# Kernel tuning notes

Measured on AMD Instinct MI355X. Metric: run time of the kernel, lower is better.

Reference implementation:

```python
import jax, jax.numpy as jnp
import numpy as np

B, S, F, H = 8, 2048, 512, 4
W = 32            # local window size
DH = F // H       # head dim
EPS = 1e-5


def layer_norm(x, w, b):
    mu = jnp.mean(x, axis=-1, keepdims=True)
    var = jnp.var(x, axis=-1, keepdims=True)
    return (x - mu) * jax.lax.rsqrt(var + EPS) * w + b


def mha(x, w_in, b_in, w_out, b_out):
    # x: [..., L, F]; torch nn.MultiheadAttention self-attention (dropout inactive / eval)
    qkv = x @ w_in.T + b_in                      # [..., L, 3F]
    q, k, v = jnp.split(qkv, 3, axis=-1)
    lead = x.shape[:-2]
    L = x.shape[-2]

    def heads(t):  # [..., L, F] -> [..., H, L, DH]
        return jnp.swapaxes(t.reshape(*lead, L, H, DH), -3, -2)

    q, k, v = heads(q), heads(k), heads(v)
    scores = jnp.einsum('...hld,...hmd->...hlm', q, k) / np.sqrt(DH)
    p = jax.nn.softmax(scores, axis=-1)
    o = jnp.einsum('...hlm,...hmd->...hld', p, v)  # [..., H, L, DH]
    o = jnp.swapaxes(o, -3, -2).reshape(*lead, L, F)
    return o @ w_out.T + b_out


def setup_inputs() -> dict:
    key = jax.random.key(0)
    ks = jax.random.split(key, 16)
    s = 0.02
    p = lambda k, shape: jax.random.normal(k, shape, dtype=jnp.float32) * s
    return {
        'x': jax.random.normal(ks[0], (B, S, F), dtype=jnp.float32),
        'l_in_w': p(ks[1], (3 * F, F)), 'l_in_b': p(ks[2], (3 * F,)),
        'l_out_w': p(ks[3], (F, F)),   'l_out_b': p(ks[4], (F,)),
        'g_in_w': p(ks[5], (3 * F, F)), 'g_in_b': p(ks[6], (3 * F,)),
        'g_out_w': p(ks[7], (F, F)),   'g_out_b': p(ks[8], (F,)),
        'n1_w': jnp.ones((F,)), 'n1_b': jnp.zeros((F,)),
        'n2_w': jnp.ones((F,)), 'n2_b': jnp.zeros((F,)),
        'gate_w': p(ks[9], (F, 2 * F)), 'gate_b': p(ks[10], (F,)),
        'gln_w': jnp.ones((F,)), 'gln_b': jnp.zeros((F,)),
    }


def reference(x, l_in_w, l_in_b, l_out_w, l_out_b,
              g_in_w, g_in_b, g_out_w, g_out_b,
              n1_w, n1_b, n2_w, n2_b,
              gate_w, gate_b, gln_w, gln_b):
    # local branch: block-diagonal (windowed) self-attention, all windows batched
    xw = x.reshape(B, S // W, W, F)
    local = mha(xw, l_in_w, l_in_b, l_out_w, l_out_b).reshape(B, S, F)
    local = layer_norm(x + local, n1_w, n1_b)
    # global branch: full self-attention
    glob = mha(x, g_in_w, g_in_b, g_out_w, g_out_b)
    glob = layer_norm(x + glob, n2_w, n2_b)
    # learned gate fusion
    gi = jnp.concatenate([local, glob], axis=-1)
    gate = jax.nn.sigmoid(layer_norm(gi @ gate_w.T + gate_b, gln_w, gln_b))
    return gate * local + (1.0 - gate) * glob
```

## Files before the change

### kernel.cpp

```cpp
#include <hip/hip_runtime.h>
#include <stdint.h>

#define BB 8
#define SS 2048
#define FF 512
#define HH 4
#define TOK (BB * SS)

typedef unsigned short u16;
typedef short short8 __attribute__((ext_vector_type(8)));
typedef float f32x4 __attribute__((ext_vector_type(4)));
typedef float f32x16 __attribute__((ext_vector_type(16)));
typedef unsigned int u32x4 __attribute__((ext_vector_type(4)));

static __device__ __forceinline__ u16 f2bf(float f) {
  uint32_t u = __builtin_bit_cast(uint32_t, f);
  u = (u + 0x7fffu + ((u >> 16) & 1u)) >> 16;
  return (u16)u;
}
static __device__ __forceinline__ float bf2f(u16 u) {
  return __builtin_bit_cast(float, (uint32_t)u << 16);
}

static __device__ __forceinline__ uint32_t cvtpk(float lo, float hi) {
  uint32_t r;
  asm("v_cvt_pk_bf16_f32 %0, %1, %2" : "=v"(r) : "v"(lo), "v"(hi));
  return r;
}

static __device__ __forceinline__ void cp16(void* lds, const void* g) {
  __builtin_amdgcn_global_load_lds(
      (const __attribute__((address_space(1))) void*)g,
      (__attribute__((address_space(3))) void*)lds, 16, 0, 0);
}

__global__ __launch_bounds__(256) void castk(const float* __restrict__ s,
                                             u16* __restrict__ d, int n) {
  const int i = (blockIdx.x * 256 + threadIdx.x) * 8;
  if (i >= n) return;
  float4 a = *(const float4*)(s + i);
  float4 b = *(const float4*)(s + i + 4);
  short8 o;
  o[0] = (short)f2bf(a.x); o[1] = (short)f2bf(a.y);
  o[2] = (short)f2bf(a.z); o[3] = (short)f2bf(a.w);
  o[4] = (short)f2bf(b.x); o[5] = (short)f2bf(b.y);
  o[6] = (short)f2bf(b.z); o[7] = (short)f2bf(b.w);
  *(short8*)(d + i) = o;
}

__global__ __launch_bounds__(256) void gemm_bt(
    const u16* __restrict__ A, const u16* __restrict__ B,
    const float* __restrict__ bias, float* __restrict__ Cf,
    u16* __restrict__ Cb, int M, int N, int K, int qcols, float qscale) {
  const int m0 = blockIdx.x << 7;
  const int n0 = blockIdx.y << 7;
  __shared__ u16 As[128 * 64];
  __shared__ u16 Bs[128 * 64];
  const int tid = threadIdx.x;
  const int wave = tid >> 6, lane = tid & 63;
  const int wr = wave >> 1, wc = wave & 1;

  f32x4 acc[4][4];
#pragma unroll
  for (int i = 0; i < 4; ++i)
#pragma unroll
    for (int j = 0; j < 4; ++j)
#pragma unroll
      for (int e = 0; e < 4; ++e) acc[i][j][e] = 0.f;

  for (int k0 = 0; k0 < K; k0 += 64) {
#pragma unroll
    for (int i = 0; i < 4; ++i) {
      const int base = (i * 4 + wave) << 10;
      const int lb = base + (lane << 4);
      const int r = lb >> 7;
      const int s = ((lb >> 4) & 7) ^ (r & 7);
      cp16((char*)As + base, A + (size_t)(m0 + r) * K + k0 + s * 8);
      cp16((char*)Bs + base, B + (size_t)(n0 + r) * K + k0 + s * 8);
    }
    __syncthreads();
#pragma unroll
    for (int kk = 0; kk < 2; ++kk) {
      short8 af[4], bfr[4];
#pragma unroll
      for (int mi = 0; mi < 4; ++mi) {
        const int r = wr * 64 + mi * 16 + (lane & 15);
        const int p = (kk * 4 + (lane >> 4)) ^ (r & 7);
        af[mi] = *(const short8*)(As + r * 64 + p * 8);
      }
#pragma unroll
      for (int ni = 0; ni < 4; ++ni) {
        const int r = wc * 64 + ni * 16 + (lane & 15);
        const int p = (kk * 4 + (lane >> 4)) ^ (r & 7);
        bfr[ni] = *(const short8*)(Bs + r * 64 + p * 8);
      }
#pragma unroll
      for (int mi = 0; mi < 4; ++mi)
#pragma unroll
        for (int ni = 0; ni < 4; ++ni)
          acc[mi][ni] = __builtin_amdgcn_mfma_f32_16x16x32_bf16(
              af[mi], bfr[ni], acc[mi][ni], 0, 0, 0);
    }
    __syncthreads();
  }
  const int rv = (lane >> 4) << 2;
  const int cn = lane & 15;
#pragma unroll
  for (int mi = 0; mi < 4; ++mi)
#pragma unroll
    for (int ni = 0; ni < 4; ++ni) {
      const int gn = n0 + wc * 64 + ni * 16 + cn;
      const float bv = bias ? bias[gn] : 0.f;
      const float sc = (gn < qcols) ? qscale : 1.f;
#pragma unroll
      for (int v = 0; v < 4; ++v) {
        const int gm = m0 + wr * 64 + mi * 16 + rv + v;
        const size_t off = (size_t)gm * N + gn;
        const float val = (acc[mi][ni][v] + bv) * sc;
        if (Cf) Cf[off] = val;
        if (Cb) Cb[off] = f2bf(val);
      }
    }
}

__global__ __launch_bounds__(256) void transpose_v(
    const u16* __restrict__ qkv, u16* __restrict__ vt) {
  const int bh = blockIdx.x, st = blockIdx.y, dt = blockIdx.z;
  const int b = bh >> 2, h = bh & 3;
  __shared__ u16 t[64][72];
  const int r = threadIdx.x >> 3;
  const int c8 = (threadIdx.x & 7) * 8;
#pragma unroll
  for (int ph = 0; ph < 2; ++ph) {
    const int srow = ph * 32 + r;
    const u16* src = qkv + (size_t)(b * SS + st * 64 + srow) * 1536 + 1024 +
                     h * 128 + dt * 64 + c8;
    *(short8*)&t[srow][c8] = *(const short8*)src;
  }
  __syncthreads();
#pragma unroll
  for (int ph = 0; ph < 2; ++ph) {
    const int drow = ph * 32 + r;
    short8 o;
#pragma unroll
    for (int j = 0; j < 8; ++j) o[j] = (short)t[c8 + j][drow];
    *(short8*)(vt + ((size_t)bh * 128 + dt * 64 + drow) * SS + st * 64 + c8) = o;
  }
}

template <typename GET>
static __device__ __forceinline__ short8 make_pa(int ks, GET get) {
  const int c0 = (2 * ks) & 3;
  u32x4 pw;
#pragma unroll
  for (int t = 0; t < 2; ++t) {
    uint32_t a = cvtpk(get(4 * c0 + 2 * t), get(4 * c0 + 2 * t + 1));
    uint32_t b = cvtpk(get(4 * (c0 + 1) + 2 * t), get(4 * (c0 + 1) + 2 * t + 1));
    auto r = __builtin_amdgcn_permlane32_swap(a, b, false, false);
    pw[t] = r[0];
    pw[2 + t] = r[1];
  }
  return __builtin_bit_cast(short8, pw);
}

__global__ __launch_bounds__(256) void attn_local(
    const u16* __restrict__ qkv, const u16* __restrict__ vt,
    u16* __restrict__ ao) {
  const int wave = threadIdx.x >> 6, lane = threadIdx.x & 63;
  const int u = blockIdx.x * 4 + wave;
  const int b = u >> 8, w = (u >> 2) & 63, h = u & 3;
  const int q = lane & 31, half = lane >> 5;

  const size_t qbase = (size_t)(b * SS + w * 32 + q) * 1536 + h * 128;
  short8 qf[8];
#pragma unroll
  for (int d8 = 0; d8 < 8; ++d8)
    qf[d8] = *(const short8*)(qkv + qbase + d8 * 16 + half * 8);

  f32x16 s;
#pragma unroll
  for (int e = 0; e < 16; ++e) s[e] = 0.f;
  const size_t kbase = qbase + 512;
#pragma unroll
  for (int d8 = 0; d8 < 8; ++d8) {
    short8 kf = *(const short8*)(qkv + kbase + d8 * 16 + half * 8);
    s = __builtin_amdgcn_mfma_f32_32x32x16_bf16(kf, qf[d8], s, 0, 0, 0);
  }
  float m = s[0];
#pragma unroll
  for (int e = 1; e < 16; ++e) m = fmaxf(m, s[e]);
  m = fmaxf(m, __shfl_xor(m, 32));
  float l = 0.f;
#pragma unroll
  for (int e = 0; e < 16; ++e) { s[e] = exp2f(s[e] - m); l += s[e]; }
  l += __shfl_xor(l, 32);

  f32x16 o[4];
#pragma unroll
  for (int nt = 0; nt < 4; ++nt)
#pragma unroll
    for (int e = 0; e < 16; ++e) o[nt][e] = 0.f;
  const size_t vbase = ((size_t)(b * 4 + h) * 128) * SS + w * 32;
#pragma unroll
  for (int ks = 0; ks < 2; ++ks) {
    short8 pa = make_pa(ks, [&](int e) { return s[e]; });
#pragma unroll
    for (int nt = 0; nt < 4; ++nt) {
      short8 vb = *(const short8*)(vt + vbase + (size_t)(nt * 32 + q) * SS +
                                   ks * 16 + half * 8);
      o[nt] = __builtin_amdgcn_mfma_f32_32x32x16_bf16(pa, vb, o[nt], 0, 0, 0);
    }
  }
  const float rl = 1.f / l;
  const size_t ob = (size_t)(b * SS + w * 32) * FF + h * 128;
#pragma unroll
  for (int e = 0; e < 16; ++e) {
    const int qr = (e & 3) + 8 * (e >> 2) + 4 * half;
    const float rf = __shfl(rl, qr);
#pragma unroll
    for (int nt = 0; nt < 4; ++nt)
      ao[ob + (size_t)qr * FF + nt * 32 + q] = f2bf(o[nt][e] * rf);
  }
}

__global__ __launch_bounds__(256) void attn_global(
    const u16* __restrict__ qkv, const u16* __restrict__ vt,
    u16* __restrict__ ao) {
  const int lb = (blockIdx.x & 7) * 64 + (blockIdx.x >> 3);
  const int bh = lb >> 4, qt = lb & 15;
  const int b = bh >> 2, h = bh & 3;
  const int wave = threadIdx.x >> 6, lane = threadIdx.x & 63;
  const int q = lane & 31, half = lane >> 5;

  __shared__ u16 Ks[2][64 * 128];
  __shared__ u16 Vs[2][128 * 64];

  short8 qf[8];
  const size_t qb = (size_t)(b * SS + qt * 128 + wave * 32 + q) * 1536 + h * 128;
#pragma unroll
  for (int d8 = 0; d8 < 8; ++d8)
    qf[d8] = *(const short8*)(qkv + qb + d8 * 16 + half * 8);

  f32x16 o[4];
#pragma unroll
  for (int nt = 0; nt < 4; ++nt)
#pragma unroll
    for (int e = 0; e < 16; ++e) o[nt][e] = 0.f;
  float m = -3e38f, lsum = 0.f;

  const size_t kbase = (size_t)b * SS * 1536 + 512 + h * 128;
  const size_t vbase = (size_t)bh * 128 * SS;

  auto STAGE = [&](int kt, int bsel) {
    u16* kd = Ks[bsel];
    u16* vd = Vs[bsel];
#pragma unroll
    for (int i = 0; i < 4; ++i) {
      const int base = (i * 4 + wave) << 10;
      const int lbk = base + (lane << 4);
      {
        const int r = lbk >> 8;
        const int sl = ((lbk >> 4) & 15) ^ (r & 7);
        cp16((char*)kd + base,
             qkv + kbase + (size_t)(kt * 64 + r) * 1536 + sl * 8);
      }
      {
        const int d = lbk >> 7;
        const int sl = ((lbk >> 4) & 7) ^ (d & 7);
        cp16((char*)vd + base, vt + vbase + (size_t)d * SS + kt * 64 + sl * 8);
      }
    }
  };
  STAGE(0, 0);
  __syncthreads();
  for (int kt = 0; kt < 32; ++kt) {
    const int cur = kt & 1;
    if (kt + 1 < 32) STAGE(kt + 1, cur ^ 1);
    const u16* Kb = Ks[cur];
    const u16* Vb = Vs[cur];

    f32x16 sa[2];
#pragma unroll
    for (int mt = 0; mt < 2; ++mt)
#pragma unroll
      for (int e = 0; e < 16; ++e) sa[mt][e] = 0.f;
    __builtin_amdgcn_s_setprio(1);
#pragma unroll
    for (int mt = 0; mt < 2; ++mt) {
      const int kr = mt * 32 + q;
#pragma unroll
      for (int d8 = 0; d8 < 8; ++d8) {
        const int ps = (d8 * 2 + half) ^ (kr & 7);
        short8 kf = *(const short8*)(Kb + kr * 128 + ps * 8);
        sa[mt] = __builtin_amdgcn_mfma_f32_32x32x16_bf16(kf, qf[d8], sa[mt], 0, 0, 0);
      }
    }
    __builtin_amdgcn_s_setprio(0);
    float t[16];
#pragma unroll
    for (int e = 0; e < 16; ++e) t[e] = fmaxf(sa[0][e], sa[1][e]);
#pragma unroll
    for (int st = 8; st >= 1; st >>= 1)
#pragma unroll
      for (int e = 0; e < 8; ++e)
        if (e < st) t[e] = fmaxf(t[e], t[e + st]);
    float pmax = fmaxf(t[0], __shfl_xor(t[0], 32));
    if (__any(pmax > m + 8.f)) {
      const float mn = fmaxf(m, pmax);
      const float corr = exp2f(m - mn);
      m = mn;
      lsum *= corr;
#pragma unroll
      for (int e = 0; e < 16; ++e) {
        const float cf = __shfl(corr, (e & 3) + 8 * (e >> 2) + 4 * half);
#pragma unroll
        for (int nt = 0; nt < 4; ++nt) o[nt][e] *= cf;
      }
    }
#pragma unroll
    for (int mt = 0; mt < 2; ++mt)
#pragma unroll
      for (int e = 0; e < 16; ++e) sa[mt][e] = exp2f(sa[mt][e] - m);
    float u[16];
#pragma unroll
    for (int e = 0; e < 16; ++e) u[e] = sa[0][e] + sa[1][e];
#pragma unroll
    for (int st = 8; st >= 1; st >>= 1)
#pragma unroll
      for (int e = 0; e < 8; ++e)
        if (e < st) u[e] += u[e + st];
    lsum += u[0] + __shfl_xor(u[0], 32);
    __builtin_amdgcn_s_setprio(1);
#pragma unroll
    for (int ks = 0; ks < 4; ++ks) {
      const int mt = ks >> 1;
      short8 pa = make_pa(ks, [&](int e) { return sa[mt][e]; });
#pragma unroll
      for (int nt = 0; nt < 4; ++nt) {
        const int d = nt * 32 + q;
        const int ps = (ks * 2 + half) ^ (d & 7);
        short8 vb = *(const short8*)(Vb + d * 64 + ps * 8);
        o[nt] = __builtin_amdgcn_mfma_f32_32x32x16_bf16(pa, vb, o[nt], 0, 0, 0);
      }
    }
    __builtin_amdgcn_s_setprio(0);
    __syncthreads();
  }
  const float rl = 1.f / lsum;
  const size_t ob = (size_t)(b * SS + qt * 128 + wave * 32) * FF + h * 128;
#pragma unroll
  for (int e = 0; e < 16; ++e) {
    const int qr = (e & 3) + 8 * (e >> 2) + 4 * half;
    const float rf = __shfl(rl, qr);
#pragma unroll
    for (int nt = 0; nt < 4; ++nt)
      ao[ob + (size_t)qr * FF + nt * 32 + q] = f2bf(o[nt][e] * rf);
  }
}

__global__ __launch_bounds__(256) void resid_ln(
    const u16* __restrict__ yb, const float* __restrict__ x,
    const float* __restrict__ w, const float* __restrict__ bv_,
    u16* __restrict__ lg) {
  const int wave = threadIdx.x >> 6, lane = threadIdx.x & 63;
  const size_t row = (size_t)blockIdx.x * 4 + wave;
  const int c = lane * 8;
  const u16* yr = yb + row * FF;
  const float* xr = x + row * FF;
  float v[8];
  {
    short8 a = *(const short8*)(yr + c);
    float4 b0 = *(const float4*)(xr + c), b1 = *(const float4*)(xr + c + 4);
    v[0] = bf2f((u16)a[0]) + b0.x; v[1] = bf2f((u16)a[1]) + b0.y;
    v[2] = bf2f((u16)a[2]) + b0.z; v[3] = bf2f((u16)a[3]) + b0.w;
    v[4] = bf2f((u16)a[4]) + b1.x; v[5] = bf2f((u16)a[5]) + b1.y;
    v[6] = bf2f((u16)a[6]) + b1.z; v[7] = bf2f((u16)a[7]) + b1.w;
  }
  float s = 0.f, s2 = 0.f;
#pragma unroll
  for (int e = 0; e < 8; ++e) { s += v[e]; s2 += v[e] * v[e]; }
#pragma unroll
  for (int off = 1; off < 64; off <<= 1) {
    s += __shfl_xor(s, off);
    s2 += __shfl_xor(s2, off);
  }
  const float mu = s * (1.f / 512.f);
  const float var = s2 * (1.f / 512.f) - mu * mu;
  const float rs = rsqrtf(var + 1e-5f);
  float4 w0 = *(const float4*)(w + c), w1 = *(const float4*)(w + c + 4);
  float4 b0 = *(const float4*)(bv_ + c), b1 = *(const float4*)(bv_ + c + 4);
  const float wv[8] = {w0.x, w0.y, w0.z, w0.w, w1.x, w1.y, w1.z, w1.w};
  const float bb[8] = {b0.x, b0.y, b0.z, b0.w, b1.x, b1.y, b1.z, b1.w};
  short8 ob;
#pragma unroll
  for (int e = 0; e < 8; ++e)
    ob[e] = (short)f2bf((v[e] - mu) * rs * wv[e] + bb[e]);
  *(short8*)(lg + row * 1024 + c) = ob;
}

__global__ __launch_bounds__(256) void gate_final(
    const float* __restrict__ gp, const u16* __restrict__ lg,
    const float* __restrict__ w, const float* __restrict__ bv_,
    float* __restrict__ out) {
  const int wave = threadIdx.x >> 6, lane = threadIdx.x & 63;
  const size_t row = (size_t)blockIdx.x * 4 + wave;
  const int c = lane * 8;
  const float* gr = gp + row * FF;
  float v[8];
  {
    float4 a0 = *(const float4*)(gr + c), a1 = *(const float4*)(gr + c + 4);
    v[0] = a0.x; v[1] = a0.y; v[2] = a0.z; v[3] = a0.w;
    v[4] = a1.x; v[5] = a1.y; v[6] = a1.z; v[7] = a1.w;
  }
  float s = 0.f, s2 = 0.f;
#pragma unroll
  for (int e = 0; e < 8; ++e) { s += v[e]; s2 += v[e] * v[e]; }
#pragma unroll
  for (int off = 1; off < 64; off <<= 1) {
    s += __shfl_xor(s, off);
    s2 += __shfl_xor(s2, off);
  }
  const float mu = s * (1.f / 512.f);
  const float var = s2 * (1.f / 512.f) - mu * mu;
  const float rs = rsqrtf(var + 1e-5f);
  float4 w0 = *(const float4*)(w + c), w1 = *(const float4*)(w + c + 4);
  float4 b0 = *(const float4*)(bv_ + c), b1 = *(const float4*)(bv_ + c + 4);
  const float wv[8] = {w0.x, w0.y, w0.z, w0.w, w1.x, w1.y, w1.z, w1.w};
  const float bb[8] = {b0.x, b0.y, b0.z, b0.w, b1.x, b1.y, b1.z, b1.w};
  short8 l8 = *(const short8*)(lg + row * 1024 + c);
  short8 g8 = *(const short8*)(lg + row * 1024 + 512 + c);
  float r[8];
#pragma unroll
  for (int e = 0; e < 8; ++e) {
    const float z = (v[e] - mu) * rs * wv[e] + bb[e];
    const float gt = 1.f / (1.f + exp2f(-1.44269504f * z));
    r[e] = gt * bf2f((u16)l8[e]) + (1.f - gt) * bf2f((u16)g8[e]);
  }
  *(float4*)(out + row * FF + c) = make_float4(r[0], r[1], r[2], r[3]);
  *(float4*)(out + row * FF + c + 4) = make_float4(r[4], r[5], r[6], r[7]);
}

extern "C" void kernel_launch(void* const* d_in, const int* in_sizes, int n_in,
                              void* d_out, int out_size, void* d_ws,
                              size_t ws_size, hipStream_t stream) {
  const float* x       = (const float*)d_in[0];
  const float* l_in_w  = (const float*)d_in[1];
  const float* l_in_b  = (const float*)d_in[2];
  const float* l_out_w = (const float*)d_in[3];
  const float* l_out_b = (const float*)d_in[4];
  const float* g_in_w  = (const float*)d_in[5];
  const float* g_in_b  = (const float*)d_in[6];
  const float* g_out_w = (const float*)d_in[7];
  const float* g_out_b = (const float*)d_in[8];
  const float* n1_w    = (const float*)d_in[9];
  const float* n1_b    = (const float*)d_in[10];
  const float* n2_w    = (const float*)d_in[11];
  const float* n2_b    = (const float*)d_in[12];
  const float* gate_w  = (const float*)d_in[13];
  const float* gate_b  = (const float*)d_in[14];
  const float* gln_w   = (const float*)d_in[15];
  const float* gln_b   = (const float*)d_in[16];
  float* out = (float*)d_out;

  const float c1 = 0.12752724808f;

  char* ws = (char*)d_ws;
  u16* x_bf  = (u16*)(ws);
  u16* w_liw = (u16*)(ws + 16777216);
  u16* w_giw = (u16*)(ws + 18350080);
  u16* w_low = (u16*)(ws + 19922944);
  u16* w_gow = (u16*)(ws + 20447232);
  u16* w_gt  = (u16*)(ws + 20971520);
  u16* qkv   = (u16*)(ws + 22020096);
  u16* vt    = (u16*)(ws + 72351744);
  u16* ato   = (u16*)(ws + 89128960);
  u16* prj   = (u16*)(ws + 105906176);
  u16* lgbf  = (u16*)(ws + 122683392);
  float* gpre = (float*)(ws + 22020096);

  castk<<<4096, 256, 0, stream>>>(x, x_bf, 8388608);
  castk<<<384, 256, 0, stream>>>(l_in_w, w_liw, 786432);
  castk<<<384, 256, 0, stream>>>(g_in_w, w_giw, 786432);
  castk<<<128, 256, 0, stream>>>(l_out_w, w_low, 262144);
  castk<<<128, 256, 0, stream>>>(g_out_w, w_gow, 262144);
  castk<<<256, 256, 0, stream>>>(gate_w, w_gt, 524288);

  gemm_bt<<<dim3(128, 12), 256, 0, stream>>>(x_bf, w_liw, l_in_b, nullptr, qkv,
                                             TOK, 1536, 512, 512, c1);
  transpose_v<<<dim3(32, 32, 2), 256, 0, stream>>>(qkv, vt);
  attn_local<<<512, 256, 0, stream>>>(qkv, vt, ato);
  gemm_bt<<<dim3(128, 4), 256, 0, stream>>>(ato, w_low, l_out_b, nullptr, prj,
                                            TOK, 512, 512, 0, 1.f);
  resid_ln<<<4096, 256, 0, stream>>>(prj, x, n1_w, n1_b, lgbf);

  gemm_bt<<<dim3(128, 12), 256, 0, stream>>>(x_bf, w_giw, g_in_b, nullptr, qkv,
                                             TOK, 1536, 512, 512, c1);
  transpose_v<<<dim3(32, 32, 2), 256, 0, stream>>>(qkv, vt);
  attn_global<<<512, 256, 0, stream>>>(qkv, vt, ato);
  gemm_bt<<<dim3(128, 4), 256, 0, stream>>>(ato, w_gow, g_out_b, nullptr, prj,
                                            TOK, 512, 512, 0, 1.f);
  resid_ln<<<4096, 256, 0, stream>>>(prj, x, n2_w, n2_b, lgbf + 512);

  gemm_bt<<<dim3(128, 4), 256, 0, stream>>>(lgbf, w_gt, gate_b, gpre, nullptr,
                                            TOK, 512, 1024, 0, 1.f);
  gate_final<<<4096, 256, 0, stream>>>(gpre, lgbf, gln_w, gln_b, out);
}
```

Before: 466.7 us.

## Fuse local and global QKV projections into one GEMM and store gate pre-activation in bf16

The local and global in-projection weights are concatenated so a single 3072-wide GEMM produces both QKV sets into one wider buffer, and all attention and transpose kernels are re-strided to read from it. This removes one kernel launch and gives the GEMM a larger grid. The gate pre-activation GEMM now writes bf16 instead of fp32, which halves that traffic but loses precision before the layer norm. The s_setprio hints around the MFMA sections in global attention are also removed.

```diff
diff --git a/kernel.cpp b/kernel.cpp
--- a/kernel.cpp
+++ b/kernel.cpp
@@ -6,6 +6,7 @@
 #define FF 512
 #define HH 4
 #define TOK (BB * SS)
+#define QST 3072
 
 typedef unsigned short u16;
 typedef short short8 __attribute__((ext_vector_type(8)));
@@ -50,8 +51,9 @@
 
 __global__ __launch_bounds__(256) void gemm_bt(
     const u16* __restrict__ A, const u16* __restrict__ B,
-    const float* __restrict__ bias, float* __restrict__ Cf,
-    u16* __restrict__ Cb, int M, int N, int K, int qcols, float qscale) {
+    const float* __restrict__ bias, const float* __restrict__ bias2,
+    u16* __restrict__ Cb, int M, int N, int K, int nsplit, int qcols,
+    float qscale) {
   const int m0 = blockIdx.x << 7;
   const int n0 = blockIdx.y << 7;
   __shared__ u16 As[128 * 64];
@@ -110,21 +112,19 @@
 #pragma unroll
     for (int ni = 0; ni < 4; ++ni) {
       const int gn = n0 + wc * 64 + ni * 16 + cn;
-      const float bv = bias ? bias[gn] : 0.f;
-      const float sc = (gn < qcols) ? qscale : 1.f;
+      const int cg = (gn >= nsplit) ? gn - nsplit : gn;
+      const float bv = (gn >= nsplit) ? bias2[cg] : bias[cg];
+      const float sc = (cg < qcols) ? qscale : 1.f;
 #pragma unroll
       for (int v = 0; v < 4; ++v) {
         const int gm = m0 + wr * 64 + mi * 16 + rv + v;
-        const size_t off = (size_t)gm * N + gn;
-        const float val = (acc[mi][ni][v] + bv) * sc;
-        if (Cf) Cf[off] = val;
-        if (Cb) Cb[off] = f2bf(val);
+        Cb[(size_t)gm * N + gn] = f2bf((acc[mi][ni][v] + bv) * sc);
       }
     }
 }
 
 __global__ __launch_bounds__(256) void transpose_v(
-    const u16* __restrict__ qkv, u16* __restrict__ vt) {
+    const u16* __restrict__ qkvp, u16* __restrict__ vt) {
   const int bh = blockIdx.x, st = blockIdx.y, dt = blockIdx.z;
   const int b = bh >> 2, h = bh & 3;
   __shared__ u16 t[64][72];
@@ -133,7 +133,7 @@
 #pragma unroll
   for (int ph = 0; ph < 2; ++ph) {
     const int srow = ph * 32 + r;
-    const u16* src = qkv + (size_t)(b * SS + st * 64 + srow) * 1536 + 1024 +
+    const u16* src = qkvp + (size_t)(b * SS + st * 64 + srow) * QST + 1024 +
                      h * 128 + dt * 64 + c8;
     *(short8*)&t[srow][c8] = *(const short8*)src;
   }
@@ -171,7 +171,7 @@
   const int b = u >> 8, w = (u >> 2) & 63, h = u & 3;
   const int q = lane & 31, half = lane >> 5;
 
-  const size_t qbase = (size_t)(b * SS + w * 32 + q) * 1536 + h * 128;
+  const size_t qbase = (size_t)(b * SS + w * 32 + q) * QST + h * 128;
   short8 qf[8];
 #pragma unroll
   for (int d8 = 0; d8 < 8; ++d8)
@@ -236,7 +236,8 @@
   __shared__ u16 Vs[2][128 * 64];
 
   short8 qf[8];
-  const size_t qb = (size_t)(b * SS + qt * 128 + wave * 32 + q) * 1536 + h * 128;
+  const size_t qb =
+      (size_t)(b * SS + qt * 128 + wave * 32 + q) * QST + 1536 + h * 128;
 #pragma unroll
   for (int d8 = 0; d8 < 8; ++d8)
     qf[d8] = *(const short8*)(qkv + qb + d8 * 16 + half * 8);
@@ -248,7 +249,7 @@
     for (int e = 0; e < 16; ++e) o[nt][e] = 0.f;
   float m = -3e38f, lsum = 0.f;
 
-  const size_t kbase = (size_t)b * SS * 1536 + 512 + h * 128;
+  const size_t kbase = (size_t)b * SS * QST + 1536 + 512 + h * 128;
   const size_t vbase = (size_t)bh * 128 * SS;
 
   auto STAGE = [&](int kt, int bsel) {
@@ -262,7 +263,7 @@
         const int r = lbk >> 8;
         const int sl = ((lbk >> 4) & 15) ^ (r & 7);
         cp16((char*)kd + base,
-             qkv + kbase + (size_t)(kt * 64 + r) * 1536 + sl * 8);
+             qkv + kbase + (size_t)(kt * 64 + r) * QST + sl * 8);
       }
       {
         const int d = lbk >> 7;
@@ -284,7 +285,6 @@
     for (int mt = 0; mt < 2; ++mt)
 #pragma unroll
       for (int e = 0; e < 16; ++e) sa[mt][e] = 0.f;
-    __builtin_amdgcn_s_setprio(1);
 #pragma unroll
     for (int mt = 0; mt < 2; ++mt) {
       const int kr = mt * 32 + q;
@@ -295,7 +295,6 @@
         sa[mt] = __builtin_amdgcn_mfma_f32_32x32x16_bf16(kf, qf[d8], sa[mt], 0, 0, 0);
       }
     }
-    __builtin_amdgcn_s_setprio(0);
     float t[16];
 #pragma unroll
     for (int e = 0; e < 16; ++e) t[e] = fmaxf(sa[0][e], sa[1][e]);
@@ -330,7 +329,6 @@
       for (int e = 0; e < 8; ++e)
         if (e < st) u[e] += u[e + st];
     lsum += u[0] + __shfl_xor(u[0], 32);
-    __builtin_amdgcn_s_setprio(1);
 #pragma unroll
     for (int ks = 0; ks < 4; ++ks) {
       const int mt = ks >> 1;
@@ -343,7 +341,6 @@
         o[nt] = __builtin_amdgcn_mfma_f32_32x32x16_bf16(pa, vb, o[nt], 0, 0, 0);
       }
     }
-    __builtin_amdgcn_s_setprio(0);
     __syncthreads();
   }
   const float rl = 1.f / lsum;
@@ -399,18 +396,17 @@
 }
 
 __global__ __launch_bounds__(256) void gate_final(
-    const float* __restrict__ gp, const u16* __restrict__ lg,
+    const u16* __restrict__ gp, const u16* __restrict__ lg,
     const float* __restrict__ w, const float* __restrict__ bv_,
     float* __restrict__ out) {
   const int wave = threadIdx.x >> 6, lane = threadIdx.x & 63;
   const size_t row = (size_t)blockIdx.x * 4 + wave;
   const int c = lane * 8;
-  const float* gr = gp + row * FF;
   float v[8];
   {
-    float4 a0 = *(const float4*)(gr + c), a1 = *(const float4*)(gr + c + 4);
-    v[0] = a0.x; v[1] = a0.y; v[2] = a0.z; v[3] = a0.w;
-    v[4] = a1.x; v[5] = a1.y; v[6] = a1.z; v[7] = a1.w;
+    short8 a = *(const short8*)(gp + row * FF + c);
+#pragma unroll
+    for (int e = 0; e < 8; ++e) v[e] = bf2f((u16)a[e]);
   }
   float s = 0.f, s2 = 0.f;
 #pragma unroll
@@ -466,42 +462,40 @@
 
   char* ws = (char*)d_ws;
   u16* x_bf  = (u16*)(ws);
-  u16* w_liw = (u16*)(ws + 16777216);
-  u16* w_giw = (u16*)(ws + 18350080);
+  u16* w_qkv = (u16*)(ws + 16777216);
   u16* w_low = (u16*)(ws + 19922944);
   u16* w_gow = (u16*)(ws + 20447232);
   u16* w_gt  = (u16*)(ws + 20971520);
-  u16* qkv   = (u16*)(ws + 22020096);
-  u16* vt    = (u16*)(ws + 72351744);
-  u16* ato   = (u16*)(ws + 89128960);
-  u16* prj   = (u16*)(ws + 105906176);
-  u16* lgbf  = (u16*)(ws + 122683392);
-  float* gpre = (float*)(ws + 22020096);
+  u16* qkv2  = (u16*)(ws + 22020096);
+  u16* vt    = (u16*)(ws + 122683392);
+  u16* ato   = (u16*)(ws + 139460608);
+  u16* prj   = (u16*)(ws + 156237824);
+  u16* lgbf  = (u16*)(ws + 173015040);
+  u16* gpre  = (u16*)(ws + 22020096);
 
   castk<<<4096, 256, 0, stream>>>(x, x_bf, 8388608);
-  castk<<<384, 256, 0, stream>>>(l_in_w, w_liw, 786432);
-  castk<<<384, 256, 0, stream>>>(g_in_w, w_giw, 786432);
+  castk<<<384, 256, 0, stream>>>(l_in_w, w_qkv, 786432);
+  castk<<<384, 256, 0, stream>>>(g_in_w, w_qkv + 786432, 786432);
   castk<<<128, 256, 0, stream>>>(l_out_w, w_low, 262144);
   castk<<<128, 256, 0, stream>>>(g_out_w, w_gow, 262144);
   castk<<<256, 256, 0, stream>>>(gate_w, w_gt, 524288);
 
-  gemm_bt<<<dim3(128, 12), 256, 0, stream>>>(x_bf, w_liw, l_in_b, nullptr, qkv,
-                                             TOK, 1536, 512, 512, c1);
-  transpose_v<<<dim3(32, 32, 2), 256, 0, stream>>>(qkv, vt);
-  attn_local<<<512, 256, 0, stream>>>(qkv, vt, ato);
-  gemm_bt<<<dim3(128, 4), 256, 0, stream>>>(ato, w_low, l_out_b, nullptr, prj,
-                                            TOK, 512, 512, 0, 1.f);
+  gemm_bt<<<dim3(128, 24), 256, 0, stream>>>(x_bf, w_qkv, l_in_b, g_in_b, qkv2,
+                                             TOK, 3072, 512, 1536, 512, c1);
+
+  transpose_v<<<dim3(32, 32, 2), 256, 0, stream>>>(qkv2, vt);
+  attn_local<<<512, 256, 0, stream>>>(qkv2, vt, ato);
+  gemm_bt<<<dim3(128, 4), 256, 0, stream>>>(ato, w_low, l_out_b, l_out_b, prj,
+                                            TOK, 512, 512, 512, 0, 1.f);
   resid_ln<<<4096, 256, 0, stream>>>(prj, x, n1_w, n1_b, lgbf);
 
-  gemm_bt<<<dim3(128, 12), 256, 0, stream>>>(x_bf, w_giw, g_in_b, nullptr, qkv,
-                                             TOK, 1536, 512, 512, c1);
-  transpose_v<<<dim3(32, 32, 2), 256, 0, stream>>>(qkv, vt);
-  attn_global<<<512, 256, 0, stream>>>(qkv, vt, ato);
-  gemm_bt<<<dim3(128, 4), 256, 0, stream>>>(ato, w_gow, g_out_b, nullptr, prj,
-                                            TOK, 512, 512, 0, 1.f);
+  transpose_v<<<dim3(32, 32, 2), 256, 0, stream>>>(qkv2 + 1536, vt);
+  attn_global<<<512, 256, 0, stream>>>(qkv2, vt, ato);
+  gemm_bt<<<dim3(128, 4), 256, 0, stream>>>(ato, w_gow, g_out_b, g_out_b, prj,
+                                            TOK, 512, 512, 512, 0, 1.f);
   resid_ln<<<4096, 256, 0, stream>>>(prj, x, n2_w, n2_b, lgbf + 512);
 
-  gemm_bt<<<dim3(128, 4), 256, 0, stream>>>(lgbf, w_gt, gate_b, gpre, nullptr,
-                                            TOK, 512, 1024, 0, 1.f);
+  gemm_bt<<<dim3(128, 4), 256, 0, stream>>>(lgbf, w_gt, gate_b, gate_b, gpre,
+                                            TOK, 512, 1024, 512, 0, 1.f);
   gate_final<<<4096, 256, 0, stream>>>(gpre, lgbf, gln_w, gln_b, out);
 }
```

After: 443.4 us. 1.05x faster.
